# Kernel tuning notes

Hardware: AMD Instinct MI355X
Metric: run time of the kernel (lower is better)

Reference implementation:

```python
import jax, jax.numpy as jnp
import numpy as np

DIM = 2048
NUM_EXPERTS = 64
NUM_TOKENS = 32768
CAPACITY_FACTOR = 1.0
EPSILON = 1e-6


def setup_inputs() -> dict:
    key = jax.random.key(0)
    k1, k2 = jax.random.split(key)
    x = jax.random.normal(k1, (NUM_TOKENS, DIM), dtype=jnp.float32)
    # nn.Linear(dim, num_experts): weight init ~ U(-1/sqrt(dim), 1/sqrt(dim))
    bound = 1.0 / np.sqrt(DIM)
    w_gate = jax.random.uniform(k2, (DIM, NUM_EXPERTS), dtype=jnp.float32,
                                minval=-bound, maxval=bound)
    b_gate = jnp.zeros((NUM_EXPERTS,), dtype=jnp.float32)
    return {"x": x, "w_gate": w_gate, "b_gate": b_gate}


def reference(x, w_gate, b_gate):
    # gate_scores = softmax(x @ W + b), shape [N, E]
    logits = jnp.einsum("nd,de->ne", x, w_gate) + b_gate
    gate_scores = jax.nn.softmax(logits, axis=-1)

    capacity = int(CAPACITY_FACTOR * x.shape[0])  # static

    # top-1 mask via argmax (equivalent to topk(1) + scatter of ones)
    top1 = jnp.argmax(gate_scores, axis=-1)                      # [N]
    mask = jax.nn.one_hot(top1, gate_scores.shape[-1],
                          dtype=gate_scores.dtype)               # [N, E]
    masked = gate_scores * mask

    # column-wise normalization, scaled by capacity
    denom = masked.sum(axis=0, keepdims=True) + EPSILON          # [1, E]
    return masked / denom * capacity
```

## Files before the change

### kernel.cpp

```cpp
#include <hip/hip_runtime.h>
#include <hip/hip_bf16.h>

#define DIM   2048
#define NEXP  64
#define NTOK  32768
#define KC    32
#define NC    (DIM / KC)
#define TB    128
#define NBLK  (NTOK / TB)
#define NSLOT 5
#define BB    12288
#define XB    16384
#define SLOTB (BB + XB)
#define WFOFF 1024

typedef __attribute__((ext_vector_type(8))) short bf16x8;
typedef __attribute__((ext_vector_type(4))) float f32x4;

typedef __attribute__((address_space(1))) const void gvoid_t;
typedef __attribute__((address_space(3))) void lvoid_t;
#define GLDS16(g, l) __builtin_amdgcn_global_load_lds((gvoid_t*)(g), (lvoid_t*)(l), 16, 0, 0)

__device__ __forceinline__ float rne_split(float v, short& h) {
    __hip_bfloat16 hb = __float2bfloat16(v);
    h = __builtin_bit_cast(short, hb);
    return __bfloat162float(hb);
}

__device__ __forceinline__ void split8(const float4& a, const float4& b,
                                       bf16x8& H, bf16x8& M, bf16x8& L) {
    const float vs[8] = {a.x, a.y, a.z, a.w, b.x, b.y, b.z, b.w};
#pragma unroll
    for (int j = 0; j < 8; ++j) {
        short h, m, l;
        const float fh = rne_split(vs[j], h);
        const float e1 = vs[j] - fh;
        const float fm = rne_split(e1, m);
        const float e2 = e1 - fm;
        rne_split(e2, l);
        H[j] = h; M[j] = m; L[j] = l;
    }
}

__global__ __launch_bounds__(256)
void wsplit_kernel(const float* __restrict__ w, bf16x8* __restrict__ wf,
                   float* __restrict__ denom) {
    if (blockIdx.x == 0 && threadIdx.x < NEXP) denom[threadIdx.x] = 0.0f;
    const int tid  = blockIdx.x * 256 + threadIdx.x;
    const int lane = tid & 63;
    const int ni   = (tid >> 6) & 3;
    const int ks   = tid >> 8;
    const int n    = ni * 16 + (lane & 15);
    const int k0   = ks * KC + (lane >> 4) * 8;
    bf16x8 H, M, L;
#pragma unroll
    for (int j = 0; j < 8; ++j) {
        const float v = w[(size_t)(k0 + j) * NEXP + n];
        short h, m, l;
        const float fh = rne_split(v, h);
        const float e1 = v - fh;
        const float fm = rne_split(e1, m);
        rne_split(e1 - fm, l);
        H[j] = h; M[j] = m; L[j] = l;
    }
    wf[((size_t)(ks * 3 + 0) * 4 + ni) * 64 + lane] = H;
    wf[((size_t)(ks * 3 + 1) * 4 + ni) * 64 + lane] = M;
    wf[((size_t)(ks * 3 + 2) * 4 + ni) * 64 + lane] = L;
}

__global__ __launch_bounds__(256, 1)
void gate_kernel(const float* __restrict__ x, const bf16x8* __restrict__ wf,
                 const float* __restrict__ b, float* __restrict__ out,
                 float* __restrict__ denom)
{
    __shared__ __align__(16) char slab[NSLOT * SLOTB];
    __shared__ float dlds[NEXP];

    const int tid  = threadIdx.x;
    const int lane = tid & 63;
    const int l15  = lane & 15;
    const int l4   = lane >> 4;
    const int wv   = tid >> 6;
    const int tok0 = blockIdx.x * TB;

    if (tid < NEXP) dlds[tid] = 0.0f;

    float bias[4];
#pragma unroll
    for (int ni = 0; ni < 4; ++ni) bias[ni] = b[ni * 16 + l15];

    const int bl0 = wv * 32 + l15;
    const int bl1 = bl0 + 16;
    const int j0  = l4 * 2;
    const int xu00 = bl0 * 8 + ((j0 + bl0) & 7);
    const int xu01 = bl0 * 8 + ((j0 + 1 + bl0) & 7);
    const int xu10 = bl1 * 8 + ((j0 + bl1) & 7);
    const int xu11 = bl1 * 8 + ((j0 + 1 + bl1) & 7);

    auto stage = [&](int slot, int c) {
        char* sb = slab + slot * SLOTB;
        const char* bsrc = (const char*)wf + (size_t)c * BB + tid * 16;
        GLDS16(bsrc,        sb + tid * 16);
        GLDS16(bsrc + 4096, sb + tid * 16 + 4096);
        GLDS16(bsrc + 8192, sb + tid * 16 + 8192);
        char* xb = sb + BB;
#pragma unroll
        for (int s = 0; s < 4; ++s) {
            const int u = s * 256 + tid;
            const int t = u >> 3;
            const int j = ((u & 7) - t) & 7;
            GLDS16(x + (size_t)(tok0 + t) * DIM + c * KC + j * 4, xb + u * 16);
        }
    };

    f32x4 acc[2][4];
#pragma unroll
    for (int mi = 0; mi < 2; ++mi)
#pragma unroll
        for (int ni = 0; ni < 4; ++ni) acc[mi][ni] = (f32x4){0.f, 0.f, 0.f, 0.f};

    stage(0, 0); stage(1, 1); stage(2, 2); stage(3, 3);

    int scomp = 0, sstage = 4;
    for (int c = 0; c < NC; ++c) {
        asm volatile("s_waitcnt vmcnt(21)" ::: "memory");
        __builtin_amdgcn_s_barrier();
        __builtin_amdgcn_sched_barrier(0);

        const char* sb = slab + scomp * SLOTB;
        const bf16x8* bl = (const bf16x8*)sb;
        bf16x8 Bf[12];
#pragma unroll
        for (int f = 0; f < 12; ++f) Bf[f] = bl[f * 64 + lane];

        const float4* xun = (const float4*)(sb + BB);
        const float4 xa0 = xun[xu00], xb0 = xun[xu01];
        const float4 xa1 = xun[xu10], xb1 = xun[xu11];

        bf16x8 Ah0, Am0, Al0, Ah1, Am1, Al1;
        split8(xa0, xb0, Ah0, Am0, Al0);
        split8(xa1, xb1, Ah1, Am1, Al1);

#pragma unroll
        for (int ni = 0; ni < 4; ++ni) {
            f32x4 a0 = acc[0][ni], a1 = acc[1][ni];
            a0 = __builtin_amdgcn_mfma_f32_16x16x32_bf16(Ah0, Bf[ni],     a0, 0, 0, 0);
            a1 = __builtin_amdgcn_mfma_f32_16x16x32_bf16(Ah1, Bf[ni],     a1, 0, 0, 0);
            a0 = __builtin_amdgcn_mfma_f32_16x16x32_bf16(Ah0, Bf[4 + ni], a0, 0, 0, 0);
            a1 = __builtin_amdgcn_mfma_f32_16x16x32_bf16(Ah1, Bf[4 + ni], a1, 0, 0, 0);
            a0 = __builtin_amdgcn_mfma_f32_16x16x32_bf16(Am0, Bf[ni],     a0, 0, 0, 0);
            a1 = __builtin_amdgcn_mfma_f32_16x16x32_bf16(Am1, Bf[ni],     a1, 0, 0, 0);
            a0 = __builtin_amdgcn_mfma_f32_16x16x32_bf16(Ah0, Bf[8 + ni], a0, 0, 0, 0);
            a1 = __builtin_amdgcn_mfma_f32_16x16x32_bf16(Ah1, Bf[8 + ni], a1, 0, 0, 0);
            a0 = __builtin_amdgcn_mfma_f32_16x16x32_bf16(Am0, Bf[4 + ni], a0, 0, 0, 0);
            a1 = __builtin_amdgcn_mfma_f32_16x16x32_bf16(Am1, Bf[4 + ni], a1, 0, 0, 0);
            a0 = __builtin_amdgcn_mfma_f32_16x16x32_bf16(Al0, Bf[ni],     a0, 0, 0, 0);
            a1 = __builtin_amdgcn_mfma_f32_16x16x32_bf16(Al1, Bf[ni],     a1, 0, 0, 0);
            acc[0][ni] = a0; acc[1][ni] = a1;
        }

        const int cn = (c + 4 < NC) ? c + 4 : NC - 1;
        stage(sstage, cn);

        if (++scomp == NSLOT) scomp = 0;
        if (++sstage == NSLOT) sstage = 0;
    }

    __syncthreads();

#pragma unroll
    for (int mi = 0; mi < 2; ++mi)
#pragma unroll
        for (int r = 0; r < 4; ++r) {
            const float v0 = acc[mi][0][r] + bias[0];
            const float v1 = acc[mi][1][r] + bias[1];
            const float v2 = acc[mi][2][r] + bias[2];
            const float v3 = acc[mi][3][r] + bias[3];

            float lm = v0; int le = l15;
            if (v1 > lm) { lm = v1; le = l15 + 16; }
            if (v2 > lm) { lm = v2; le = l15 + 32; }
            if (v3 > lm) { lm = v3; le = l15 + 48; }
#pragma unroll
            for (int off = 1; off < 16; off <<= 1) {
                const float om = __shfl_xor(lm, off);
                const int   oe = __shfl_xor(le, off);
                if (om > lm || (om == lm && oe < le)) { lm = om; le = oe; }
            }
            float s = __expf(v0 - lm) + __expf(v1 - lm) +
                      __expf(v2 - lm) + __expf(v3 - lm);
#pragma unroll
            for (int off = 1; off < 16; off <<= 1) s += __shfl_xor(s, off);
            const float g = 1.0f / s;

            const int t = tok0 + wv * 32 + mi * 16 + 4 * l4 + r;
            float* orow = out + (size_t)t * NEXP + l15;
            orow[0]  = (le == l15     ) ? g : 0.0f;
            orow[16] = (le == l15 + 16) ? g : 0.0f;
            orow[32] = (le == l15 + 32) ? g : 0.0f;
            orow[48] = (le == l15 + 48) ? g : 0.0f;
            if (l15 == 0) atomicAdd(&dlds[le], g);
        }

    __syncthreads();
    if (tid < NEXP) atomicAdd(&denom[tid], dlds[tid]);
}

__global__ __launch_bounds__(256)
void scale_kernel(float* __restrict__ out, const float* __restrict__ denom)
{
    __shared__ float sc[NEXP];
    if (threadIdx.x < NEXP)
        sc[threadIdx.x] = (float)NTOK / (denom[threadIdx.x] + 1e-6f);
    __syncthreads();

    const size_t i = (size_t)blockIdx.x * blockDim.x + threadIdx.x;
    float4 v = ((const float4*)out)[i];
    const int e0 = (int)((i * 4) & (NEXP - 1));
    v.x *= sc[e0]; v.y *= sc[e0 + 1]; v.z *= sc[e0 + 2]; v.w *= sc[e0 + 3];
    ((float4*)out)[i] = v;
}

extern "C" void kernel_launch(void* const* d_in, const int* in_sizes, int n_in,
                              void* d_out, int out_size, void* d_ws, size_t ws_size,
                              hipStream_t stream) {
    const float* x = (const float*)d_in[0];
    const float* w = (const float*)d_in[1];
    const float* b = (const float*)d_in[2];
    float*  out   = (float*)d_out;
    float*  denom = (float*)d_ws;
    bf16x8* wf    = (bf16x8*)((char*)d_ws + WFOFF);

    wsplit_kernel<<<64, 256, 0, stream>>>(w, wf, denom);
    gate_kernel<<<NBLK, 256, 0, stream>>>(x, wf, b, out, denom);
    scale_kernel<<<(NTOK * NEXP / 4) / 256, 256, 0, stream>>>(out, denom);
}
```

Baseline: 81.46 us.

## Load x straight into registers with double buffering, stage only weights in LDS

Activation tiles no longer go through LDS via global_load_lds. Each lane now reads its own x rows straight into registers, two K-chunks ahead, using two alternating register buffers, and the main loop is unrolled by two. Only the pre-split weight fragments still use the 5-slot LDS ring, which cuts the shared-memory footprint and removes the LDS write/read round trip for x. The price is more live vector registers, a hand-tuned vmcnt wait that must match the new load ordering, and direct global reads of 32-byte row segments with a large stride, which may coalesce less well.

```diff
diff --git a/kernel.cpp b/kernel.cpp
--- a/kernel.cpp
+++ b/kernel.cpp
@@ -5,13 +5,11 @@
 #define NEXP  64
 #define NTOK  32768
 #define KC    32
-#define NC    (DIM / KC)
+#define NC    64
 #define TB    128
 #define NBLK  (NTOK / TB)
 #define NSLOT 5
 #define BB    12288
-#define XB    16384
-#define SLOTB (BB + XB)
 #define WFOFF 1024
 
 typedef __attribute__((ext_vector_type(8))) short bf16x8;
@@ -73,7 +71,7 @@
                  const float* __restrict__ b, float* __restrict__ out,
                  float* __restrict__ denom)
 {
-    __shared__ __align__(16) char slab[NSLOT * SLOTB];
+    __shared__ __align__(16) char slab[NSLOT * BB];
     __shared__ float dlds[NEXP];
 
     const int tid  = threadIdx.x;
@@ -89,29 +87,21 @@
 #pragma unroll
     for (int ni = 0; ni < 4; ++ni) bias[ni] = b[ni * 16 + l15];
 
-    const int bl0 = wv * 32 + l15;
-    const int bl1 = bl0 + 16;
-    const int j0  = l4 * 2;
-    const int xu00 = bl0 * 8 + ((j0 + bl0) & 7);
-    const int xu01 = bl0 * 8 + ((j0 + 1 + bl0) & 7);
-    const int xu10 = bl1 * 8 + ((j0 + bl1) & 7);
-    const int xu11 = bl1 * 8 + ((j0 + 1 + bl1) & 7);
-
-    auto stage = [&](int slot, int c) {
-        char* sb = slab + slot * SLOTB;
-        const char* bsrc = (const char*)wf + (size_t)c * BB + tid * 16;
-        GLDS16(bsrc,        sb + tid * 16);
-        GLDS16(bsrc + 4096, sb + tid * 16 + 4096);
-        GLDS16(bsrc + 8192, sb + tid * 16 + 8192);
-        char* xb = sb + BB;
-#pragma unroll
-        for (int s = 0; s < 4; ++s) {
-            const int u = s * 256 + tid;
-            const int t = u >> 3;
-            const int j = ((u & 7) - t) & 7;
-            GLDS16(x + (size_t)(tok0 + t) * DIM + c * KC + j * 4, xb + u * 16);
-        }
-    };
+    const float* xr0 = x + (size_t)(tok0 + wv * 32 + l15) * DIM + l4 * 8;
+    const float* xr1 = xr0 + (size_t)16 * DIM;
+
+#define LOADX(X, c) {                                                  \
+    X[0] = *(const float4*)(xr0 + (size_t)(c) * KC);                   \
+    X[1] = *(const float4*)(xr0 + (size_t)(c) * KC + 4);               \
+    X[2] = *(const float4*)(xr1 + (size_t)(c) * KC);                   \
+    X[3] = *(const float4*)(xr1 + (size_t)(c) * KC + 4); }
+
+#define STAGE(slot, c) {                                               \
+    const char* _src = (const char*)wf + (size_t)(c) * BB + tid * 16;  \
+    char* _dst = slab + (size_t)(slot) * BB + tid * 16;                \
+    GLDS16(_src, _dst);                                                \
+    GLDS16(_src + 4096, _dst + 4096);                                  \
+    GLDS16(_src + 8192, _dst + 8192); }
 
     f32x4 acc[2][4];
 #pragma unroll
@@ -119,53 +109,69 @@
 #pragma unroll
         for (int ni = 0; ni < 4; ++ni) acc[mi][ni] = (f32x4){0.f, 0.f, 0.f, 0.f};
 
-    stage(0, 0); stage(1, 1); stage(2, 2); stage(3, 3);
+    float4 xa[4], xb[4];
+    STAGE(0, 0)
+    __builtin_amdgcn_sched_barrier(0);
+    STAGE(1, 1)
+    __builtin_amdgcn_sched_barrier(0);
+    LOADX(xa, 0)
+    __builtin_amdgcn_sched_barrier(0);
+    STAGE(2, 2)
+    __builtin_amdgcn_sched_barrier(0);
+    LOADX(xb, 1)
+    __builtin_amdgcn_sched_barrier(0);
+    STAGE(3, 3)
+    __builtin_amdgcn_sched_barrier(0);
+
+#define ITER(c, scomp, sstage, XC) {                                   \
+    asm volatile("s_waitcnt vmcnt(10)" ::: "memory");                  \
+    __builtin_amdgcn_s_barrier();                                      \
+    __builtin_amdgcn_sched_barrier(0);                                 \
+    const bf16x8* _bl = (const bf16x8*)(slab + (size_t)(scomp) * BB);  \
+    bf16x8 Bf[12];                                                     \
+    _Pragma("unroll")                                                  \
+    for (int _f = 0; _f < 12; ++_f) Bf[_f] = _bl[_f * 64 + lane];      \
+    __builtin_amdgcn_sched_barrier(0);                                 \
+    bf16x8 Ah0, Am0, Al0, Ah1, Am1, Al1;                               \
+    split8(XC[0], XC[1], Ah0, Am0, Al0);                               \
+    split8(XC[2], XC[3], Ah1, Am1, Al1);                               \
+    __builtin_amdgcn_sched_barrier(0);                                 \
+    { const int _cx = ((c) + 2 < NC) ? (c) + 2 : NC - 1;               \
+      LOADX(XC, _cx) }                                                 \
+    __builtin_amdgcn_sched_barrier(0);                                 \
+    { const int _cs = ((c) + 4 < NC) ? (c) + 4 : NC - 1;               \
+      STAGE(sstage, _cs) }                                             \
+    __builtin_amdgcn_sched_barrier(0);                                 \
+    _Pragma("unroll")                                                  \
+    for (int _ni = 0; _ni < 4; ++_ni) {                                \
+        f32x4 _a0 = acc[0][_ni], _a1 = acc[1][_ni];                    \
+        _a0 = __builtin_amdgcn_mfma_f32_16x16x32_bf16(Ah0, Bf[_ni],     _a0, 0, 0, 0); \
+        _a1 = __builtin_amdgcn_mfma_f32_16x16x32_bf16(Ah1, Bf[_ni],     _a1, 0, 0, 0); \
+        _a0 = __builtin_amdgcn_mfma_f32_16x16x32_bf16(Ah0, Bf[4 + _ni], _a0, 0, 0, 0); \
+        _a1 = __builtin_amdgcn_mfma_f32_16x16x32_bf16(Ah1, Bf[4 + _ni], _a1, 0, 0, 0); \
+        _a0 = __builtin_amdgcn_mfma_f32_16x16x32_bf16(Am0, Bf[_ni],     _a0, 0, 0, 0); \
+        _a1 = __builtin_amdgcn_mfma_f32_16x16x32_bf16(Am1, Bf[_ni],     _a1, 0, 0, 0); \
+        _a0 = __builtin_amdgcn_mfma_f32_16x16x32_bf16(Ah0, Bf[8 + _ni], _a0, 0, 0, 0); \
+        _a1 = __builtin_amdgcn_mfma_f32_16x16x32_bf16(Ah1, Bf[8 + _ni], _a1, 0, 0, 0); \
+        _a0 = __builtin_amdgcn_mfma_f32_16x16x32_bf16(Am0, Bf[4 + _ni], _a0, 0, 0, 0); \
+        _a1 = __builtin_amdgcn_mfma_f32_16x16x32_bf16(Am1, Bf[4 + _ni], _a1, 0, 0, 0); \
+        _a0 = __builtin_amdgcn_mfma_f32_16x16x32_bf16(Al0, Bf[_ni],     _a0, 0, 0, 0); \
+        _a1 = __builtin_amdgcn_mfma_f32_16x16x32_bf16(Al1, Bf[_ni],     _a1, 0, 0, 0); \
+        acc[0][_ni] = _a0; acc[1][_ni] = _a1;                          \
+    } }
 
     int scomp = 0, sstage = 4;
-    for (int c = 0; c < NC; ++c) {
-        asm volatile("s_waitcnt vmcnt(21)" ::: "memory");
-        __builtin_amdgcn_s_barrier();
-        __builtin_amdgcn_sched_barrier(0);
-
-        const char* sb = slab + scomp * SLOTB;
-        const bf16x8* bl = (const bf16x8*)sb;
-        bf16x8 Bf[12];
-#pragma unroll
-        for (int f = 0; f < 12; ++f) Bf[f] = bl[f * 64 + lane];
-
-        const float4* xun = (const float4*)(sb + BB);
-        const float4 xa0 = xun[xu00], xb0 = xun[xu01];
-        const float4 xa1 = xun[xu10], xb1 = xun[xu11];
-
-        bf16x8 Ah0, Am0, Al0, Ah1, Am1, Al1;
-        split8(xa0, xb0, Ah0, Am0, Al0);
-        split8(xa1, xb1, Ah1, Am1, Al1);
-
-#pragma unroll
-        for (int ni = 0; ni < 4; ++ni) {
-            f32x4 a0 = acc[0][ni], a1 = acc[1][ni];
-            a0 = __builtin_amdgcn_mfma_f32_16x16x32_bf16(Ah0, Bf[ni],     a0, 0, 0, 0);
-            a1 = __builtin_amdgcn_mfma_f32_16x16x32_bf16(Ah1, Bf[ni],     a1, 0, 0, 0);
-            a0 = __builtin_amdgcn_mfma_f32_16x16x32_bf16(Ah0, Bf[4 + ni], a0, 0, 0, 0);
-            a1 = __builtin_amdgcn_mfma_f32_16x16x32_bf16(Ah1, Bf[4 + ni], a1, 0, 0, 0);
-            a0 = __builtin_amdgcn_mfma_f32_16x16x32_bf16(Am0, Bf[ni],     a0, 0, 0, 0);
-            a1 = __builtin_amdgcn_mfma_f32_16x16x32_bf16(Am1, Bf[ni],     a1, 0, 0, 0);
-            a0 = __builtin_amdgcn_mfma_f32_16x16x32_bf16(Ah0, Bf[8 + ni], a0, 0, 0, 0);
-            a1 = __builtin_amdgcn_mfma_f32_16x16x32_bf16(Ah1, Bf[8 + ni], a1, 0, 0, 0);
-            a0 = __builtin_amdgcn_mfma_f32_16x16x32_bf16(Am0, Bf[4 + ni], a0, 0, 0, 0);
-            a1 = __builtin_amdgcn_mfma_f32_16x16x32_bf16(Am1, Bf[4 + ni], a1, 0, 0, 0);
-            a0 = __builtin_amdgcn_mfma_f32_16x16x32_bf16(Al0, Bf[ni],     a0, 0, 0, 0);
-            a1 = __builtin_amdgcn_mfma_f32_16x16x32_bf16(Al1, Bf[ni],     a1, 0, 0, 0);
-            acc[0][ni] = a0; acc[1][ni] = a1;
-        }
-
-        const int cn = (c + 4 < NC) ? c + 4 : NC - 1;
-        stage(sstage, cn);
-
+#pragma unroll 1
+    for (int c = 0; c < NC; c += 2) {
+        ITER(c, scomp, sstage, xa)
+        if (++scomp == NSLOT) scomp = 0;
+        if (++sstage == NSLOT) sstage = 0;
+        ITER(c + 1, scomp, sstage, xb)
         if (++scomp == NSLOT) scomp = 0;
         if (++sstage == NSLOT) sstage = 0;
     }
 
+    asm volatile("s_waitcnt vmcnt(0)" ::: "memory");
     __syncthreads();
 
 #pragma unroll
```

Result: slower. 87.61 us (+7.6%).
